# Performance work log

Hardware: AMD Instinct MI355X
Metric: run time of the kernel (lower is better)

## Reference

```python
import jax, jax.numpy as jnp
import numpy as np

B, S, F, D = 64, 129, 768, 4
MOM = 0.9
EPS = 1e-6


def setup_inputs() -> dict:
    key = jax.random.key(0)
    ks = jax.random.split(key, 8)
    x = jax.random.normal(ks[0], (B, S, F), dtype=jnp.float32)
    labels = jax.random.randint(ks[1], (B,), 0, 16, dtype=jnp.int32)
    domain = jax.random.randint(ks[2], (B,), 0, D, dtype=jnp.int32)
    lmda = jax.random.beta(ks[3], 0.1, 0.1, (B, 1, 1)).astype(jnp.float32)
    d_rand = jax.random.randint(ks[4], (B,), 1, D, dtype=jnp.int32)  # range(1, num_domains)
    mean_buf = (0.1 * jax.random.normal(ks[5], (D, F))).astype(jnp.float32)
    var_buf = jax.random.uniform(ks[6], (D, F), minval=0.5, maxval=1.5, dtype=jnp.float32)
    hg_noise = jax.random.normal(ks[7], (B, S, F), dtype=jnp.float32)
    return {"input": x, "lmda": lmda, "mean_buf": mean_buf, "var_buf": var_buf,
            "hg_noise": hg_noise, "labels": labels, "domain": domain, "d_rand": d_rand}


def reference(input, lmda, mean_buf, var_buf, hg_noise, labels, domain, d_rand):
    x = input  # [B,S,F]
    b, s, f = x.shape
    d = mean_buf.shape[0]

    # --- per-domain mean/var over dims [0,1] (unbiased), momentum buffer update ---
    tok = x.reshape(b * s, f)
    seg = jnp.repeat(domain, s)  # [B*S]
    cnt = jax.ops.segment_sum(jnp.ones((b * s,), x.dtype), seg, num_segments=d)  # tokens/domain
    s1 = jax.ops.segment_sum(tok, seg, num_segments=d)          # [D,F]
    s2 = jax.ops.segment_sum(tok * tok, seg, num_segments=d)    # [D,F]
    n = cnt[:, None]
    mu_d = s1 / jnp.maximum(n, 1.0)
    var_d = (s2 - n * mu_d * mu_d) / jnp.maximum(n - 1.0, 1.0)  # unbiased, matches torch.var
    present = (cnt > 0)[:, None]
    new_mean = jnp.where(present, MOM * mean_buf + (1.0 - MOM) * mu_d, mean_buf)
    new_var = jnp.where(present, MOM * var_buf + (1.0 - MOM) * var_d, var_buf)

    # --- instance renorm over token dim (unbiased var) + cross-domain restyle ---
    mu_i = x.mean(1, keepdims=True)
    v_i = x.var(1, keepdims=True, ddof=1)
    x_normed = (x - mu_i) * jax.lax.rsqrt(v_i + EPS)
    ds = (domain + d_rand) % d
    x_new = x_normed * jnp.sqrt(new_var[ds] + EPS)[:, None, :] + new_mean[ds][:, None, :]
    x_mix = lmda * x + (1.0 - lmda) * x_new

    # --- Gaussian hallucinated samples from own-domain stats ---
    hg = new_mean[domain][:, None, :] + jnp.sqrt(new_var[domain] + EPS)[:, None, :] * hg_noise

    # --- pairwise euclidean distance + hard example mining + soft-margin triplet loss ---
    xe = jnp.concatenate([x, x_mix, hg], axis=0).reshape(3 * b, s * f)  # [3B, S*F]
    ln = jnp.concatenate([labels, labels, -jnp.ones((b,), labels.dtype)])
    sq = jnp.sum(xe * xe, axis=1)
    d2 = sq[:, None] + sq[None, :] - 2.0 * (xe @ xe.T)
    dist = jnp.sqrt(jnp.clip(d2, 1e-12))
    pos = ln[:, None] == ln[None, :]
    big = jnp.asarray(1e30, dist.dtype)
    dist_ap = jnp.max(jnp.where(pos, dist, -big), axis=1)
    dist_an = jnp.min(jnp.where(pos, big, dist), axis=1)
    tri_hard_loss = jnp.mean(jax.nn.softplus(dist_ap - dist_an))  # SoftMarginLoss, y=1

    return x_mix, tri_hard_loss, new_mean, new_var
```

## Files before the change

kernel.cpp:

```cpp
#include <hip/hip_runtime.h>
#include <math.h>

#define B_ 64
#define S_ 129
#define F_ 768
#define N3 192
#define BF 49152
#define NCHUNK 1548
#define GMAIN 256
#define GSZ 36864

#define WS_NM   0
#define WS_SV   3072
#define WS_C1   6144
#define WS_C0   55296
#define WS_HGM  104448
#define WS_HGS  153600
#define WS_S1   202752
#define WS_S2   251904
#define WS_PART 337920

#define OUT_LOSS 6340608
#define OUT_NM   6340609
#define OUT_NV   6343681

typedef unsigned int uint;
using short8v = __attribute__((ext_vector_type(8))) short;
using float4v = __attribute__((ext_vector_type(4))) float;

__global__ void k_stats(const float* __restrict__ x,
                        float* __restrict__ s1, float* __restrict__ s2) {
    __shared__ float4 r1[256], r2[256];
    int b = blockIdx.x / 3, fg = blockIdx.x % 3;
    int c = threadIdx.x & 63, sp = threadIdx.x >> 6;
    int f = fg * 256 + c * 4;
    const float* p = x + (size_t)b * S_ * F_ + f;
    int s0 = sp * 32;
    int se = s0 + 32 + (sp == 3 ? 1 : 0);
    float4 a1 = {0.f,0.f,0.f,0.f}, a2 = {0.f,0.f,0.f,0.f};
#pragma unroll 4
    for (int s = s0; s < se; ++s) {
        float4 v = *(const float4*)(p + s * F_);
        a1.x += v.x; a1.y += v.y; a1.z += v.z; a1.w += v.w;
        a2.x += v.x*v.x; a2.y += v.y*v.y; a2.z += v.z*v.z; a2.w += v.w*v.w;
    }
    r1[threadIdx.x] = a1; r2[threadIdx.x] = a2;
    __syncthreads();
    if (sp == 0) {
        float4 t1 = r1[c], t2 = r2[c];
#pragma unroll
        for (int k = 1; k < 4; ++k) {
            float4 u1 = r1[k * 64 + c], u2 = r2[k * 64 + c];
            t1.x += u1.x; t1.y += u1.y; t1.z += u1.z; t1.w += u1.w;
            t2.x += u2.x; t2.y += u2.y; t2.z += u2.z; t2.w += u2.w;
        }
        *(float4*)(s1 + b * F_ + f) = t1;
        *(float4*)(s2 + b * F_ + f) = t2;
    }
}

__global__ void k_dom(const float* __restrict__ s1, const float* __restrict__ s2,
                      const int* __restrict__ domain,
                      const float* __restrict__ mean_buf, const float* __restrict__ var_buf,
                      float* __restrict__ nm_tab, float* __restrict__ sv_tab,
                      float* __restrict__ out_nm, float* __restrict__ out_nv) {
    int idx = blockIdx.x * 256 + threadIdx.x;
    if (idx >= F_ * 4) return;
    int f = idx >> 2, d = idx & 3;
    float a1 = 0.f, a2 = 0.f, cntf = 0.f;
#pragma unroll 8
    for (int b = 0; b < B_; ++b) {
        float v1 = s1[b * F_ + f];
        float v2 = s2[b * F_ + f];
        bool mk = (domain[b] == d);
        a1 += mk ? v1 : 0.0f;
        a2 += mk ? v2 : 0.0f;
        cntf += mk ? 1.0f : 0.0f;
    }
    float nm, nv;
    if (cntf > 0.f) {
        float n = cntf * (float)S_;
        float mu = a1 / n;
        float var = (a2 - n * mu * mu) / fmaxf(n - 1.0f, 1.0f);
        nm = 0.9f * mean_buf[d * F_ + f] + 0.1f * mu;
        nv = 0.9f * var_buf[d * F_ + f] + 0.1f * var;
    } else {
        nm = mean_buf[d * F_ + f];
        nv = var_buf[d * F_ + f];
    }
    out_nm[d * F_ + f] = nm;
    out_nv[d * F_ + f] = nv;
    nm_tab[d * F_ + f] = nm;
    sv_tab[d * F_ + f] = sqrtf(nv + 1e-6f);
}

__global__ void k_coef(const float* __restrict__ s1, const float* __restrict__ s2,
                       const float* __restrict__ lmda,
                       const int* __restrict__ domain, const int* __restrict__ d_rand,
                       const float* __restrict__ nm_tab, const float* __restrict__ sv_tab,
                       float* __restrict__ c1, float* __restrict__ c0,
                       float* __restrict__ hgm, float* __restrict__ hgs,
                       float* __restrict__ out_loss) {
    int t = blockIdx.x * 256 + threadIdx.x;
    if (blockIdx.x == 0 && threadIdx.x == 0) out_loss[0] = 0.0f;
    int b = t / F_, f = t - b * F_;
    float mu = s1[t] * (1.0f / (float)S_);
    float v  = (s2[t] - (float)S_ * mu * mu) * (1.0f / (float)(S_ - 1));
    float r  = rsqrtf(v + 1e-6f);
    int dm = domain[b];
    int ds = (dm + d_rand[b]) & 3;
    float sv = sv_tab[ds * F_ + f];
    float nm = nm_tab[ds * F_ + f];
    float lam = lmda[b];
    float rs = r * sv;
    c1[t] = lam + (1.0f - lam) * rs;
    c0[t] = (1.0f - lam) * (nm - mu * rs);
    hgm[t] = nm_tab[dm * F_ + f];
    hgs[t] = sv_tab[dm * F_ + f];
}

__device__ __forceinline__ uint pack2(float a, float b) {
    uint ua = __float_as_uint(a);
    uint ub = __float_as_uint(b);
    uint ha = (ua + 0x7FFFu + ((ua >> 16) & 1u)) >> 16;
    uint hb = (ub + 0x7FFFu + ((ub >> 16) & 1u)) & 0xFFFF0000u;
    return hb | ha;
}

__device__ __forceinline__ void bf16_store8(char* lds, int row, int g,
                                            float4 v0, float4 v1) {
    uint4 H;
    H.x = pack2(v0.x, v0.y);
    H.y = pack2(v0.z, v0.w);
    H.z = pack2(v1.x, v1.y);
    H.w = pack2(v1.z, v1.w);
    *(uint4*)(lds + row * 128 + ((g ^ (row & 7)) << 4)) = H;
}

__device__ __forceinline__ float4 fma4(float4 a, float4 x, float4 b) {
    float4 r;
    r.x = fmaf(a.x, x.x, b.x); r.y = fmaf(a.y, x.y, b.y);
    r.z = fmaf(a.z, x.z, b.z); r.w = fmaf(a.w, x.w, b.w);
    return r;
}

template <bool EXCL>
__global__ __launch_bounds__(512, 2)
void k_main(const float* __restrict__ x, const float* __restrict__ hgn,
            const float* __restrict__ c1, const float* __restrict__ c0,
            const float* __restrict__ hgm, const float* __restrict__ hgs,
            float* __restrict__ xmix, float* part, int npart) {
    __shared__ __align__(16) char LDS[24576];
    float4v acc[6][3];
#pragma unroll
    for (int i = 0; i < 6; ++i)
#pragma unroll
        for (int j = 0; j < 3; ++j)
            acc[i][j] = (float4v){0.f, 0.f, 0.f, 0.f};

    int tid = threadIdx.x;
    int b = tid >> 3;
    int g = tid & 7;
    int w = tid >> 6;
    int wr = (w >> 2) * 96, wc = (w & 3) * 48;
    int lane = tid & 63, m = lane & 15, qd = lane >> 4;

    int q = blockIdx.x;
    size_t goff; int cb;
    {
        int s = q / 12, f0 = (q - s * 12) * 64;
        goff = ((size_t)b * S_ + s) * F_ + f0 + (g << 3);
        cb = b * F_ + f0 + (g << 3);
    }
    float4 X0 = ((const float4*)(x + goff))[0];
    float4 X1 = ((const float4*)(x + goff))[1];
    float4 N0 = ((const float4*)(hgn + goff))[0];
    float4 N1 = ((const float4*)(hgn + goff))[1];
    float4 C1a = ((const float4*)(c1 + cb))[0], C1b = ((const float4*)(c1 + cb))[1];
    float4 C0a = ((const float4*)(c0 + cb))[0], C0b = ((const float4*)(c0 + cb))[1];
    float4 HMa = ((const float4*)(hgm + cb))[0], HMb = ((const float4*)(hgm + cb))[1];
    float4 HSa = ((const float4*)(hgs + cb))[0], HSb = ((const float4*)(hgs + cb))[1];

    for (; q < NCHUNK; q += GMAIN) {
        float4 M0 = fma4(C1a, X0, C0a);
        float4 M1 = fma4(C1b, X1, C0b);
        ((float4*)(xmix + goff))[0] = M0;
        ((float4*)(xmix + goff))[1] = M1;
        float4 H0 = fma4(HSa, N0, HMa);
        float4 H1 = fma4(HSb, N1, HMb);

        bf16_store8(LDS, b, g, X0, X1);
        bf16_store8(LDS, 64 + b, g, M0, M1);
        bf16_store8(LDS, 128 + b, g, H0, H1);
        __syncthreads();

        int qn = q + GMAIN;
        if (qn < NCHUNK) {
            int s = qn / 12, f0 = (qn - s * 12) * 64;
            goff = ((size_t)b * S_ + s) * F_ + f0 + (g << 3);
            cb = b * F_ + f0 + (g << 3);
            X0 = ((const float4*)(x + goff))[0];
            X1 = ((const float4*)(x + goff))[1];
            N0 = ((const float4*)(hgn + goff))[0];
            N1 = ((const float4*)(hgn + goff))[1];
            C1a = ((const float4*)(c1 + cb))[0]; C1b = ((const float4*)(c1 + cb))[1];
            C0a = ((const float4*)(c0 + cb))[0]; C0b = ((const float4*)(c0 + cb))[1];
            HMa = ((const float4*)(hgm + cb))[0]; HMb = ((const float4*)(hgm + cb))[1];
            HSa = ((const float4*)(hgs + cb))[0]; HSb = ((const float4*)(hgs + cb))[1];
        }

#pragma unroll
        for (int t = 0; t < 2; ++t) {
            short8v A[6];
#pragma unroll
            for (int i = 0; i < 6; ++i) {
                int row = wr + i * 16 + m;
                int go = (((t << 2) + qd) ^ (row & 7)) << 4;
                A[i] = *(const short8v*)(LDS + row * 128 + go);
            }
#pragma unroll
            for (int j = 0; j < 3; ++j) {
                int row = wc + j * 16 + m;
                int go = (((t << 2) + qd) ^ (row & 7)) << 4;
                short8v Bv = *(const short8v*)(LDS + row * 128 + go);
#pragma unroll
                for (int i = 0; i < 6; ++i)
                    acc[i][j] = __builtin_amdgcn_mfma_f32_16x16x32_bf16(A[i], Bv, acc[i][j], 0, 0, 0);
            }
        }
        __syncthreads();
    }

    float* dst = part + (size_t)(blockIdx.x % npart) * GSZ;
#pragma unroll
    for (int i = 0; i < 6; ++i)
#pragma unroll
        for (int j = 0; j < 3; ++j) {
            int base = (wr + i * 16 + qd * 4) * N3 + wc + j * 16 + m;
#pragma unroll
            for (int r = 0; r < 4; ++r) {
                int o = base + r * N3;
                if (EXCL) dst[o] = acc[i][j][r];
                else atomicAdd(dst + o, acc[i][j][r]);
            }
        }
}

__global__ void k_red(const float* __restrict__ part, float* __restrict__ gram, int npart) {
    int j = blockIdx.x * 256 + threadIdx.x;
    float s = 0.0f;
#pragma unroll 8
    for (int p = 0; p < npart; ++p) s += part[(size_t)p * GSZ + j];
    gram[j] = s;
}

__global__ void k_loss(const float* __restrict__ gram, const int* __restrict__ labels,
                       float* __restrict__ out_loss) {
    __shared__ float sq[N3];
    __shared__ int ln[N3];
    int i = blockIdx.x, lane = threadIdx.x;
    for (int k = lane; k < N3; k += 64) {
        sq[k] = gram[k * (N3 + 1)];
        ln[k] = (k < 128) ? labels[k & 63] : -1;
    }
    __syncthreads();
    int li = ln[i];
    float si = sq[i];
    float ap = -1e30f, an = 1e30f;
    for (int j = lane; j < N3; j += 64) {
        float d2 = si + sq[j] - 2.0f * gram[i * N3 + j];
        float dist = sqrtf(fmaxf(d2, 1e-12f));
        bool pos = (li == ln[j]);
        ap = pos ? fmaxf(ap, dist) : ap;
        an = pos ? an : fminf(an, dist);
    }
#pragma unroll
    for (int off = 32; off; off >>= 1) {
        ap = fmaxf(ap, __shfl_xor(ap, off));
        an = fminf(an, __shfl_xor(an, off));
    }
    if (lane == 0) {
        float xv = ap - an;
        float sp = fmaxf(xv, 0.0f) + log1pf(expf(-fabsf(xv)));
        atomicAdd(out_loss, sp * (1.0f / (float)N3));
    }
}

extern "C" void kernel_launch(void* const* d_in, const int* in_sizes, int n_in,
                              void* d_out, int out_size, void* d_ws, size_t ws_size,
                              hipStream_t stream) {
    const float* x        = (const float*)d_in[0];
    const float* lmda     = (const float*)d_in[1];
    const float* mean_buf = (const float*)d_in[2];
    const float* var_buf  = (const float*)d_in[3];
    const float* hgn      = (const float*)d_in[4];
    const int*   labels   = (const int*)d_in[5];
    const int*   domain   = (const int*)d_in[6];
    const int*   d_rand   = (const int*)d_in[7];
    float* out = (float*)d_out;
    float* ws  = (float*)d_ws;

    long avail = (long)(ws_size / 4) - WS_PART;
    int npart = (int)(avail / GSZ) - 1;
    if (npart < 1) npart = 1;
    if (npart > GMAIN) npart = GMAIN;
    bool excl = (npart == GMAIN);
    float* part = ws + WS_PART;
    float* gram = ws + WS_PART + (size_t)npart * GSZ;

    k_stats<<<dim3(192), dim3(256), 0, stream>>>(x, ws + WS_S1, ws + WS_S2);
    k_dom<<<dim3(12), dim3(256), 0, stream>>>(ws + WS_S1, ws + WS_S2, domain,
                                              mean_buf, var_buf,
                                              ws + WS_NM, ws + WS_SV,
                                              out + OUT_NM, out + OUT_NV);
    k_coef<<<dim3(192), dim3(256), 0, stream>>>(ws + WS_S1, ws + WS_S2, lmda,
                                                domain, d_rand,
                                                ws + WS_NM, ws + WS_SV,
                                                ws + WS_C1, ws + WS_C0,
                                                ws + WS_HGM, ws + WS_HGS,
                                                out + OUT_LOSS);
    if (!excl) {
        hipMemsetAsync(part, 0, (size_t)npart * GSZ * 4, stream);
    }
    if (excl) {
        k_main<true><<<dim3(GMAIN), dim3(512), 0, stream>>>(
            x, hgn, ws + WS_C1, ws + WS_C0, ws + WS_HGM, ws + WS_HGS,
            out, part, npart);
    } else {
        k_main<false><<<dim3(GMAIN), dim3(512), 0, stream>>>(
            x, hgn, ws + WS_C1, ws + WS_C0, ws + WS_HGM, ws + WS_HGS,
            out, part, npart);
    }
    k_red<<<dim3(144), dim3(256), 0, stream>>>(part, gram, npart);
    k_loss<<<dim3(N3), dim3(64), 0, stream>>>(gram, labels, out + OUT_LOSS);
}
```

Baseline: 160.1 us.

## Fuse domain-stats and coefficient kernels into main Gram kernel with fixed feature-column blocks

Removes the k_dom and k_coef launches. Each main block now owns one 64-wide feature column and iterates over tokens with stride 21, so it computes its domain mean/var tables and per-batch coefficients once in LDS and registers, with no per-chunk coefficient reloads. The partial-Gram write-out is staged through LDS so it leaves as coalesced float4 stores instead of scattered scalar stores. Grid drops to 252 blocks, and each block redundantly recomputes the domain reductions over s1/s2 for its column.

```diff
diff --git a/kernel.cpp b/kernel.cpp
--- a/kernel.cpp
+++ b/kernel.cpp
@@ -5,20 +5,12 @@
 #define S_ 129
 #define F_ 768
 #define N3 192
-#define BF 49152
-#define NCHUNK 1548
-#define GMAIN 256
 #define GSZ 36864
-
-#define WS_NM   0
-#define WS_SV   3072
-#define WS_C1   6144
-#define WS_C0   55296
-#define WS_HGM  104448
-#define WS_HGS  153600
-#define WS_S1   202752
-#define WS_S2   251904
-#define WS_PART 337920
+#define GRID_MAIN 252
+
+#define WS_S1   0
+#define WS_S2   49152
+#define WS_PART 98304
 
 #define OUT_LOSS 6340608
 #define OUT_NM   6340609
@@ -29,8 +21,10 @@
 using float4v = __attribute__((ext_vector_type(4))) float;
 
 __global__ void k_stats(const float* __restrict__ x,
-                        float* __restrict__ s1, float* __restrict__ s2) {
+                        float* __restrict__ s1, float* __restrict__ s2,
+                        float* __restrict__ out_loss) {
     __shared__ float4 r1[256], r2[256];
+    if (blockIdx.x == 0 && threadIdx.x == 0) out_loss[0] = 0.0f;
     int b = blockIdx.x / 3, fg = blockIdx.x % 3;
     int c = threadIdx.x & 63, sp = threadIdx.x >> 6;
     int f = fg * 256 + c * 4;
@@ -59,66 +53,6 @@
     }
 }
 
-__global__ void k_dom(const float* __restrict__ s1, const float* __restrict__ s2,
-                      const int* __restrict__ domain,
-                      const float* __restrict__ mean_buf, const float* __restrict__ var_buf,
-                      float* __restrict__ nm_tab, float* __restrict__ sv_tab,
-                      float* __restrict__ out_nm, float* __restrict__ out_nv) {
-    int idx = blockIdx.x * 256 + threadIdx.x;
-    if (idx >= F_ * 4) return;
-    int f = idx >> 2, d = idx & 3;
-    float a1 = 0.f, a2 = 0.f, cntf = 0.f;
-#pragma unroll 8
-    for (int b = 0; b < B_; ++b) {
-        float v1 = s1[b * F_ + f];
-        float v2 = s2[b * F_ + f];
-        bool mk = (domain[b] == d);
-        a1 += mk ? v1 : 0.0f;
-        a2 += mk ? v2 : 0.0f;
-        cntf += mk ? 1.0f : 0.0f;
-    }
-    float nm, nv;
-    if (cntf > 0.f) {
-        float n = cntf * (float)S_;
-        float mu = a1 / n;
-        float var = (a2 - n * mu * mu) / fmaxf(n - 1.0f, 1.0f);
-        nm = 0.9f * mean_buf[d * F_ + f] + 0.1f * mu;
-        nv = 0.9f * var_buf[d * F_ + f] + 0.1f * var;
-    } else {
-        nm = mean_buf[d * F_ + f];
-        nv = var_buf[d * F_ + f];
-    }
-    out_nm[d * F_ + f] = nm;
-    out_nv[d * F_ + f] = nv;
-    nm_tab[d * F_ + f] = nm;
-    sv_tab[d * F_ + f] = sqrtf(nv + 1e-6f);
-}
-
-__global__ void k_coef(const float* __restrict__ s1, const float* __restrict__ s2,
-                       const float* __restrict__ lmda,
-                       const int* __restrict__ domain, const int* __restrict__ d_rand,
-                       const float* __restrict__ nm_tab, const float* __restrict__ sv_tab,
-                       float* __restrict__ c1, float* __restrict__ c0,
-                       float* __restrict__ hgm, float* __restrict__ hgs,
-                       float* __restrict__ out_loss) {
-    int t = blockIdx.x * 256 + threadIdx.x;
-    if (blockIdx.x == 0 && threadIdx.x == 0) out_loss[0] = 0.0f;
-    int b = t / F_, f = t - b * F_;
-    float mu = s1[t] * (1.0f / (float)S_);
-    float v  = (s2[t] - (float)S_ * mu * mu) * (1.0f / (float)(S_ - 1));
-    float r  = rsqrtf(v + 1e-6f);
-    int dm = domain[b];
-    int ds = (dm + d_rand[b]) & 3;
-    float sv = sv_tab[ds * F_ + f];
-    float nm = nm_tab[ds * F_ + f];
-    float lam = lmda[b];
-    float rs = r * sv;
-    c1[t] = lam + (1.0f - lam) * rs;
-    c0[t] = (1.0f - lam) * (nm - mu * rs);
-    hgm[t] = nm_tab[dm * F_ + f];
-    hgs[t] = sv_tab[dm * F_ + f];
-}
-
 __device__ __forceinline__ uint pack2(float a, float b) {
     uint ua = __float_as_uint(a);
     uint ub = __float_as_uint(b);
@@ -147,41 +81,99 @@
 template <bool EXCL>
 __global__ __launch_bounds__(512, 2)
 void k_main(const float* __restrict__ x, const float* __restrict__ hgn,
-            const float* __restrict__ c1, const float* __restrict__ c0,
-            const float* __restrict__ hgm, const float* __restrict__ hgs,
-            float* __restrict__ xmix, float* part, int npart) {
-    __shared__ __align__(16) char LDS[24576];
-    float4v acc[6][3];
-#pragma unroll
-    for (int i = 0; i < 6; ++i)
-#pragma unroll
-        for (int j = 0; j < 3; ++j)
-            acc[i][j] = (float4v){0.f, 0.f, 0.f, 0.f};
+            const float* __restrict__ s1, const float* __restrict__ s2,
+            const float* __restrict__ mean_buf, const float* __restrict__ var_buf,
+            const float* __restrict__ lmda, const int* __restrict__ domain,
+            const int* __restrict__ d_rand,
+            float* __restrict__ xmix, float* __restrict__ out_nm,
+            float* __restrict__ out_nv,
+            float* part, int npart) {
+    __shared__ __align__(16) char LDS[25088];
+    __shared__ float NMV[4][64];
+    __shared__ float SVV[4][64];
 
     int tid = threadIdx.x;
-    int b = tid >> 3;
-    int g = tid & 7;
+    int bid = blockIdx.x;
+    int fc = bid % 12, sb = bid / 12;
+    int f0 = fc * 64;
+    int b = tid >> 3, g = tid & 7;
     int w = tid >> 6;
     int wr = (w >> 2) * 96, wc = (w & 3) * 48;
     int lane = tid & 63, m = lane & 15, qd = lane >> 4;
 
-    int q = blockIdx.x;
-    size_t goff; int cb;
-    {
-        int s = q / 12, f0 = (q - s * 12) * 64;
-        goff = ((size_t)b * S_ + s) * F_ + f0 + (g << 3);
-        cb = b * F_ + f0 + (g << 3);
-    }
+    int s = sb;
+    size_t goff = ((size_t)b * S_ + s) * F_ + f0 + (g << 3);
     float4 X0 = ((const float4*)(x + goff))[0];
     float4 X1 = ((const float4*)(x + goff))[1];
     float4 N0 = ((const float4*)(hgn + goff))[0];
     float4 N1 = ((const float4*)(hgn + goff))[1];
-    float4 C1a = ((const float4*)(c1 + cb))[0], C1b = ((const float4*)(c1 + cb))[1];
-    float4 C0a = ((const float4*)(c0 + cb))[0], C0b = ((const float4*)(c0 + cb))[1];
-    float4 HMa = ((const float4*)(hgm + cb))[0], HMb = ((const float4*)(hgm + cb))[1];
-    float4 HSa = ((const float4*)(hgs + cb))[0], HSb = ((const float4*)(hgs + cb))[1];
-
-    for (; q < NCHUNK; q += GMAIN) {
+
+    if (tid < 256) {
+        int d = tid & 3, fl = tid >> 2;
+        int f = f0 + fl;
+        float a1 = 0.f, a2 = 0.f, cnt = 0.f;
+#pragma unroll 8
+        for (int bb = 0; bb < B_; ++bb) {
+            bool mk = (domain[bb] == d);
+            a1  += mk ? s1[bb * F_ + f] : 0.f;
+            a2  += mk ? s2[bb * F_ + f] : 0.f;
+            cnt += mk ? 1.f : 0.f;
+        }
+        float nm, nv;
+        if (cnt > 0.f) {
+            float n = cnt * (float)S_;
+            float mu = a1 / n;
+            float var = (a2 - n * mu * mu) / fmaxf(n - 1.f, 1.f);
+            nm = 0.9f * mean_buf[d * F_ + f] + 0.1f * mu;
+            nv = 0.9f * var_buf[d * F_ + f] + 0.1f * var;
+        } else {
+            nm = mean_buf[d * F_ + f];
+            nv = var_buf[d * F_ + f];
+        }
+        NMV[d][fl] = nm;
+        SVV[d][fl] = sqrtf(nv + 1e-6f);
+        if (sb == 0) { out_nm[d * F_ + f] = nm; out_nv[d * F_ + f] = nv; }
+    }
+    __syncthreads();
+
+    int cb = b * F_ + f0 + (g << 3);
+    float4 S1a = ((const float4*)(s1 + cb))[0], S1b = ((const float4*)(s1 + cb))[1];
+    float4 S2a = ((const float4*)(s2 + cb))[0], S2b = ((const float4*)(s2 + cb))[1];
+    int dm = domain[b];
+    int dsd = (dm + d_rand[b]) & 3;
+    float lam = lmda[b];
+    float4 C1a, C1b, C0a, C0b, HMa, HMb, HSa, HSb;
+#define COEF(SC1, SC2, FL, RC1, RC0, RHM, RHS) {            \
+        float mu = (SC1) * (1.0f / (float)S_);              \
+        float v  = ((SC2) - (float)S_ * mu * mu) * (1.0f / (float)(S_ - 1)); \
+        float r  = rsqrtf(v + 1e-6f);                       \
+        float sv = SVV[dsd][FL];                            \
+        float rs = r * sv;                                  \
+        RC1 = lam + (1.0f - lam) * rs;                      \
+        RC0 = (1.0f - lam) * (NMV[dsd][FL] - mu * rs);      \
+        RHM = NMV[dm][FL];                                  \
+        RHS = SVV[dm][FL]; }
+    {
+        int fb = g << 3;
+        COEF(S1a.x, S2a.x, fb + 0, C1a.x, C0a.x, HMa.x, HSa.x);
+        COEF(S1a.y, S2a.y, fb + 1, C1a.y, C0a.y, HMa.y, HSa.y);
+        COEF(S1a.z, S2a.z, fb + 2, C1a.z, C0a.z, HMa.z, HSa.z);
+        COEF(S1a.w, S2a.w, fb + 3, C1a.w, C0a.w, HMa.w, HSa.w);
+        COEF(S1b.x, S2b.x, fb + 4, C1b.x, C0b.x, HMb.x, HSb.x);
+        COEF(S1b.y, S2b.y, fb + 5, C1b.y, C0b.y, HMb.y, HSb.y);
+        COEF(S1b.z, S2b.z, fb + 6, C1b.z, C0b.z, HMb.z, HSb.z);
+        COEF(S1b.w, S2b.w, fb + 7, C1b.w, C0b.w, HMb.w, HSb.w);
+    }
+#undef COEF
+
+    float4v acc[6][3];
+#pragma unroll
+    for (int i = 0; i < 6; ++i)
+#pragma unroll
+        for (int j = 0; j < 3; ++j)
+            acc[i][j] = (float4v){0.f, 0.f, 0.f, 0.f};
+
+    for (; s < S_; s += 21) {
         float4 M0 = fma4(C1a, X0, C0a);
         float4 M1 = fma4(C1b, X1, C0b);
         ((float4*)(xmix + goff))[0] = M0;
@@ -194,19 +186,13 @@
         bf16_store8(LDS, 128 + b, g, H0, H1);
         __syncthreads();
 
-        int qn = q + GMAIN;
-        if (qn < NCHUNK) {
-            int s = qn / 12, f0 = (qn - s * 12) * 64;
-            goff = ((size_t)b * S_ + s) * F_ + f0 + (g << 3);
-            cb = b * F_ + f0 + (g << 3);
+        int sn = s + 21;
+        if (sn < S_) {
+            goff = ((size_t)b * S_ + sn) * F_ + f0 + (g << 3);
             X0 = ((const float4*)(x + goff))[0];
             X1 = ((const float4*)(x + goff))[1];
             N0 = ((const float4*)(hgn + goff))[0];
             N1 = ((const float4*)(hgn + goff))[1];
-            C1a = ((const float4*)(c1 + cb))[0]; C1b = ((const float4*)(c1 + cb))[1];
-            C0a = ((const float4*)(c0 + cb))[0]; C0b = ((const float4*)(c0 + cb))[1];
-            HMa = ((const float4*)(hgm + cb))[0]; HMb = ((const float4*)(hgm + cb))[1];
-            HSa = ((const float4*)(hgs + cb))[0]; HSb = ((const float4*)(hgs + cb))[1];
         }
 
 #pragma unroll
@@ -231,19 +217,38 @@
         __syncthreads();
     }
 
-    float* dst = part + (size_t)(blockIdx.x % npart) * GSZ;
-#pragma unroll
-    for (int i = 0; i < 6; ++i)
+    float* T = (float*)LDS;
+    const int PADW = 196;
+    float* dst = part + (size_t)(bid % npart) * GSZ;
+    int lrb = (wr ? 16 : 0) + (qd << 2);
+    int lr2 = tid >> 4;
+#pragma unroll
+    for (int i = 0; i < 6; ++i) {
+        __syncthreads();
 #pragma unroll
         for (int j = 0; j < 3; ++j) {
-            int base = (wr + i * 16 + qd * 4) * N3 + wc + j * 16 + m;
-#pragma unroll
-            for (int r = 0; r < 4; ++r) {
-                int o = base + r * N3;
-                if (EXCL) dst[o] = acc[i][j][r];
-                else atomicAdd(dst + o, acc[i][j][r]);
+            int colb = wc + j * 16 + m;
+#pragma unroll
+            for (int r = 0; r < 4; ++r)
+                T[(lrb + r) * PADW + colb] = acc[i][j][r];
+        }
+        __syncthreads();
+        int grow = i * 16 + (lr2 & 15) + (lr2 >> 4) * 96;
+#pragma unroll
+        for (int k = 0; k < 3; ++k) {
+            int c4 = k * 16 + (tid & 15);
+            float4 vv = *(const float4*)&T[lr2 * PADW + (c4 << 2)];
+            int o = grow * N3 + (c4 << 2);
+            if (EXCL) {
+                *(float4*)(dst + o) = vv;
+            } else {
+                atomicAdd(dst + o + 0, vv.x);
+                atomicAdd(dst + o + 1, vv.y);
+                atomicAdd(dst + o + 2, vv.z);
+                atomicAdd(dst + o + 3, vv.w);
             }
         }
+    }
 }
 
 __global__ void k_red(const float* __restrict__ part, float* __restrict__ gram, int npart) {
@@ -303,33 +308,26 @@
     long avail = (long)(ws_size / 4) - WS_PART;
     int npart = (int)(avail / GSZ) - 1;
     if (npart < 1) npart = 1;
-    if (npart > GMAIN) npart = GMAIN;
-    bool excl = (npart == GMAIN);
+    if (npart > GRID_MAIN) npart = GRID_MAIN;
+    bool excl = (npart == GRID_MAIN);
     float* part = ws + WS_PART;
     float* gram = ws + WS_PART + (size_t)npart * GSZ;
 
-    k_stats<<<dim3(192), dim3(256), 0, stream>>>(x, ws + WS_S1, ws + WS_S2);
-    k_dom<<<dim3(12), dim3(256), 0, stream>>>(ws + WS_S1, ws + WS_S2, domain,
-                                              mean_buf, var_buf,
-                                              ws + WS_NM, ws + WS_SV,
-                                              out + OUT_NM, out + OUT_NV);
-    k_coef<<<dim3(192), dim3(256), 0, stream>>>(ws + WS_S1, ws + WS_S2, lmda,
-                                                domain, d_rand,
-                                                ws + WS_NM, ws + WS_SV,
-                                                ws + WS_C1, ws + WS_C0,
-                                                ws + WS_HGM, ws + WS_HGS,
-                                                out + OUT_LOSS);
+    k_stats<<<dim3(192), dim3(256), 0, stream>>>(x, ws + WS_S1, ws + WS_S2,
+                                                 out + OUT_LOSS);
     if (!excl) {
         hipMemsetAsync(part, 0, (size_t)npart * GSZ * 4, stream);
     }
     if (excl) {
-        k_main<true><<<dim3(GMAIN), dim3(512), 0, stream>>>(
-            x, hgn, ws + WS_C1, ws + WS_C0, ws + WS_HGM, ws + WS_HGS,
-            out, part, npart);
+        k_main<true><<<dim3(GRID_MAIN), dim3(512), 0, stream>>>(
+            x, hgn, ws + WS_S1, ws + WS_S2, mean_buf, var_buf,
+            lmda, domain, d_rand,
+            out, out + OUT_NM, out + OUT_NV, part, npart);
     } else {
-        k_main<false><<<dim3(GMAIN), dim3(512), 0, stream>>>(
-            x, hgn, ws + WS_C1, ws + WS_C0, ws + WS_HGM, ws + WS_HGS,
-            out, part, npart);
+        k_main<false><<<dim3(GRID_MAIN), dim3(512), 0, stream>>>(
+            x, hgn, ws + WS_S1, ws + WS_S2, mean_buf, var_buf,
+            lmda, domain, d_rand,
+            out, out + OUT_NM, out + OUT_NV, part, npart);
     }
     k_red<<<dim3(144), dim3(256), 0, stream>>>(part, gram, npart);
     k_loss<<<dim3(N3), dim3(64), 0, stream>>>(gram, labels, out + OUT_LOSS);
```

Measured after the change: 154.2 us. 1.04x faster.
